# Performance work log

Measured on AMD Instinct MI355X. Metric: run time of the kernel, lower is better.

## Reference

```python
import jax, jax.numpy as jnp
import numpy as np

B, H, W = 4, 512, 512
NOI = 4
LMBDA = 1.0
RHO = 1.0
ALPHA = 1.8
MU = 1.0
C = RHO / (MU + RHO)

QTAB = np.array([16,11,10,16,24,40,51,61,
                 12,12,14,19,26,58,60,55,
                 14,13,16,24,40,57,69,56,
                 14,17,22,29,51,87,80,62,
                 18,22,37,56,68,109,103,77,
                 24,35,55,64,81,104,113,92,
                 49,64,78,87,103,121,120,101,
                 72,92,95,98,112,100,103,99], dtype=np.float32) / 255.0

def _dct_basis():
    xs = 2.0 * np.arange(8) + 1.0
    us = np.pi * np.arange(8) / 16.0
    a = np.ones(8, np.float64); a[0] = 1.0 / np.sqrt(2.0)
    cos = np.cos(np.outer(xs, us)) * a[None, :]          # [x, u]
    F = 0.25 * np.einsum('xu,yv->xyuv', cos, cos).reshape(8, 8, 64)
    return jnp.asarray(F, jnp.float32)

F_DCT = _dct_basis()                                     # [8,8,64]
Q = jnp.asarray(QTAB).reshape(1, 1, 1, 64)

# tf.image kernels (rows index input channel)
K_RGB2YUV = jnp.array([[0.299, -0.14714119, 0.61497538],
                       [0.587, -0.28886916, -0.51496512],
                       [0.114,  0.43601035, -0.10001026]], jnp.float32)
K_YUV2RGB = jnp.array([[1.0, 1.0, 1.0],
                       [0.0, -0.394642334, 2.03206185],
                       [1.13988303, -0.58062185, 0.0]], jnp.float32)

def _dct_blocks(x):
    # x: [B,h*8,w*8] single channel -> [B,h,w,64]; equals stride-8 conv with DCT filters
    b, hh, ww = x.shape
    blk = x.reshape(b, hh // 8, 8, ww // 8, 8)
    return jnp.einsum('bhiwj,ijk->bhwk', blk, F_DCT)

def _idct_blocks(c):
    # c: [B,h,w,64] -> [B,h*8,w*8]; equals depth_to_space + IDCT conv + depth_to_space
    b, hh, ww, _ = c.shape
    img = jnp.einsum('bhwk,ijk->bhiwj', c, F_DCT)
    return img.reshape(b, hh * 8, ww * 8)

def _W(rgb):
    # RGB2JPEG_Coef: rgb -> (y_coefs, u_coefs, v_coefs)
    yuv = rgb @ K_RGB2YUV
    y = yuv[..., 0] - 0.5
    u, v = yuv[..., 1], yuv[..., 2]
    def ds(t):  # 2x2 average pool
        b, hh, ww = t.shape
        return t.reshape(b, hh // 2, 2, ww // 2, 2).mean(axis=(2, 4))
    return (_dct_blocks(y), _dct_blocks(ds(u)), _dct_blocks(ds(v)))

def _Wt(coefs):
    # JPEG_Coef2RGB: (y_c, u_c, v_c) -> rgb
    yc, uc, vc = coefs
    y = jnp.clip(_idct_blocks(yc) + 0.5, 0.0, 1.0)
    def up(t):
        return jnp.repeat(jnp.repeat(t, 2, axis=1), 2, axis=2)
    u = jnp.clip(up(_idct_blocks(uc)), -0.5, 0.5)
    v = jnp.clip(up(_idct_blocks(vc)), -0.5, 0.5)
    yuv = jnp.stack([y, u, v], axis=-1)
    return jnp.clip(yuv @ K_YUV2RGB, 0.0, 1.0)

def _quant_adjust(Wx, r):
    # QuantizationAdjustment: piecewise-best of 3 candidates, elementwise
    y = Wx + C * r
    ry = Q * jnp.round(y / Q)
    sgn_r = jnp.sign(r)
    hqm = Q / 2 - 1.0 / 510.0
    hqp = Q / 2 + 1.0 / 510.0
    def err(d):
        return (MU / 2) * jnp.square(C * r + d) + \
               (RHO / 2) * jnp.square(-MU / (MU + RHO) + Q * jnp.round((y + d) / Q) - y)
    c1 = -sgn_r * jnp.minimum(C * jnp.abs(r), jnp.abs(ry - y - sgn_r * Q * hqm))
    c2 = ry - hqp * Q * jnp.sign(y - ry - C * r) - y
    c3 = -sgn_r * jnp.minimum(C * jnp.abs(r), jnp.abs(ry - y - sgn_r * Q * (1.0 + hqm)))
    best = jnp.where(err(c2) < err(c1), c2, c1)
    return jnp.where(err(c3) < err(best), c3, best)

def _forward(img):
    hh, ww = img.shape[1], img.shape[2]
    # XUpdate: FFT-domain proxy solve with filters [0,1] (vertical / horizontal)
    k1 = jnp.zeros((hh, ww), jnp.float32).at[1, 0].set(1.0)
    k2 = jnp.zeros((hh, ww), jnp.float32).at[0, 1].set(1.0)
    F1 = jnp.fft.rfft2(k1)
    F2 = jnp.fft.rfft2(k2)
    A = 1.0 + LMBDA * (jnp.abs(F1) ** 2 + jnp.abs(F2) ** 2)  # [H, W//2+1]
    def xup(t):
        Tf = jnp.fft.rfft2(t, axes=(1, 2))
        return jnp.fft.irfft2(Tf / A[None, :, :, None], s=(hh, ww), axes=(1, 2))

    Ws = _W(img)
    negC = tuple(Q * jnp.round(w / Q) for w in Ws)
    y = img
    By = negC
    u = tuple(jnp.zeros_like(w) for w in Ws)

    for _ in range(NOI):
        x = xup(y)
        AxplusC = tuple((1.0 - ALPHA) * By[c] - (2.0 - ALPHA) * negC[c] for c in range(3))
        Wx = _W(x)
        r = tuple(-AxplusC[c] - Wx[c] - u[c] for c in range(3))
        Wdz = tuple(_quant_adjust(Wx[c], r[c]) for c in range(3))
        y = x + C * _Wt(r) + _Wt(Wdz)
        By = tuple(Q * jnp.round((Wx[c] + C * r[c] + Wdz[c]) / Q) for c in range(3))
        u = tuple(u[c] + AxplusC[c] + By[c] for c in range(3))

    return xup(y)

def setup_inputs() -> dict:
    key = jax.random.key(0)
    s = jax.random.uniform(key, (B, H, W, 3), dtype=jnp.float32)
    return {"s": s}

def reference(s) -> jnp.ndarray:
    return _forward(s)
```

## Files before the change

kernel.cpp:

```cpp
#include <hip/hip_runtime.h>
#include <math.h>

#define H1 0.49039264020161522f
#define H2 0.46193976625564338f
#define H3 0.41573480615127262f
#define H4 0.35355339059327376f
#define H5 0.27778511650980111f
#define H6 0.19134171618254489f
#define H7 0.09754516100806413f

__device__ __constant__ float cBB[64] = {
  H4,  H1,  H2,  H3,  H4,  H5,  H6,  H7,
  H4,  H3,  H6, -H7, -H4, -H1, -H2, -H5,
  H4,  H5, -H6, -H1, -H4,  H7,  H2,  H3,
  H4,  H7, -H2, -H5,  H4,  H3, -H6, -H1,
  H4, -H7, -H2,  H5,  H4, -H3, -H6,  H1,
  H4, -H5, -H6,  H1, -H4, -H7,  H2, -H3,
  H4, -H3,  H6,  H7, -H4,  H1, -H2,  H5,
  H4, -H1,  H2, -H3,  H4, -H5,  H6, -H7,
};

__device__ __constant__ float cQ[64] = {
  16.f/255.f, 11.f/255.f, 10.f/255.f, 16.f/255.f, 24.f/255.f, 40.f/255.f, 51.f/255.f, 61.f/255.f,
  12.f/255.f, 12.f/255.f, 14.f/255.f, 19.f/255.f, 26.f/255.f, 58.f/255.f, 60.f/255.f, 55.f/255.f,
  14.f/255.f, 13.f/255.f, 16.f/255.f, 24.f/255.f, 40.f/255.f, 57.f/255.f, 69.f/255.f, 56.f/255.f,
  14.f/255.f, 17.f/255.f, 22.f/255.f, 29.f/255.f, 51.f/255.f, 87.f/255.f, 80.f/255.f, 62.f/255.f,
  18.f/255.f, 22.f/255.f, 37.f/255.f, 56.f/255.f, 68.f/255.f, 109.f/255.f, 103.f/255.f, 77.f/255.f,
  24.f/255.f, 35.f/255.f, 55.f/255.f, 64.f/255.f, 81.f/255.f, 104.f/255.f, 113.f/255.f, 92.f/255.f,
  49.f/255.f, 64.f/255.f, 78.f/255.f, 87.f/255.f, 103.f/255.f, 121.f/255.f, 120.f/255.f, 101.f/255.f,
  72.f/255.f, 92.f/255.f, 95.f/255.f, 98.f/255.f, 112.f/255.f, 100.f/255.f, 103.f/255.f, 99.f/255.f,
};

__device__ __forceinline__ float clampf(float x, float lo, float hi) {
    return fminf(fmaxf(x, lo), hi);
}
__device__ __forceinline__ float sgnf(float x) {
    return (x > 0.f) ? 1.f : ((x < 0.f) ? -1.f : 0.f);
}
__device__ __forceinline__ void wave_fence() {
    asm volatile("" ::: "memory");
    __builtin_amdgcn_wave_barrier();
}

__global__ __launch_bounds__(128, 4)
void smooth_jpeg_kernel(const float* __restrict__ s, float* __restrict__ out)
{
    const int t  = threadIdx.x;
    const int l  = t & 63;
    const int w  = t >> 6;
    const int li = l >> 3, lj = l & 7;

    const int tile = blockIdx.x;
    const int bb = tile >> 10;
    const int ti = tile & 1023;
    const int ty = (ti >> 5) * 16;
    const int tx = (ti & 31) * 16;

    __shared__ __align__(16) float BBr[64];
    __shared__ __align__(16) float BBt[64];
    __shared__ __align__(16) float lya[2][128];
    __shared__ __align__(16) float lyb[2][128];
    __shared__ __align__(16) float cuv[2][2][64];
    __shared__ __align__(16) float cst[2][128];
    __shared__ __align__(16) float cb[256];

    if (t < 64) { BBr[t] = cBB[t]; BBt[t] = cBB[(t & 7)*8 + (t >> 3)]; }

    const int gy = ty + w*8 + li;
    int pixo[2];
    float yrv[2], ygv[2], ybv[2];
    #pragma unroll
    for (int k = 0; k < 2; ++k) {
        pixo[k] = ((bb*512 + gy)*512 + (tx + k*8 + lj))*3;
        yrv[k] = s[pixo[k]+0];
        ygv[k] = s[pixo[k]+1];
        ybv[k] = s[pixo[k]+2];
    }

    const float q     = cQ[l];
    const float hqm   = 0.5f*q - (1.0f/510.0f);
    const float qhqm1 = q * hqm;
    const float qhqm3 = q * (1.0f + hqm);
    const float qhqp  = (0.5f*q + (1.0f/510.0f)) * q;

    const bool pooler = ((l & 9) == 0);

    auto load8 = [](const float* p, float* d) {
        float4 a = *reinterpret_cast<const float4*>(p);
        float4 c = *reinterpret_cast<const float4*>(p + 4);
        d[0]=a.x; d[1]=a.y; d[2]=a.z; d[3]=a.w;
        d[4]=c.x; d[5]=c.y; d[6]=c.z; d[7]=c.w;
    };

    auto phaseA = [&](const float* pr, const float* pg, const float* pb,
                      float* pY, int par) {
        #pragma unroll
        for (int k = 0; k < 2; ++k) {
            float yv = 0.299f*pr[k] + 0.587f*pg[k] + 0.114f*pb[k] - 0.5f;
            float uu = -0.14714119f*pr[k] - 0.28886916f*pg[k] + 0.43601035f*pb[k];
            float vv =  0.61497538f*pr[k] - 0.51496512f*pg[k] - 0.10001026f*pb[k];
            pY[k] = yv;
            float ub = __shfl_xor(uu,1), uc = __shfl_xor(uu,8), ud = __shfl_xor(uu,9);
            float vb = __shfl_xor(vv,1), vc = __shfl_xor(vv,8), vd = __shfl_xor(vv,9);
            if (pooler) {
                int ci = (w*4 + (li>>1))*8 + k*4 + (lj>>1);
                cuv[par][0][ci] = 0.25f * (((uu + ub) + uc) + ud);
                cuv[par][1][ci] = 0.25f * (((vv + vb) + vc) + vd);
            }
        }
    };

    auto fwdAll = [&](const float* pY, float* wy, float& wc, int par) {
        #pragma unroll
        for (int k = 0; k < 2; ++k) lya[w][k*64 + l] = pY[k];
        wave_fence();
        float bt[8]; load8(&BBt[lj*8], bt);
        float rs[2], rsc;
        #pragma unroll
        for (int k = 0; k < 2; ++k) {
            float c8[8]; load8(&lya[w][k*64 + li*8], c8);
            float a = 0.f;
            #pragma unroll
            for (int j = 0; j < 8; ++j) a = fmaf(c8[j], bt[j], a);
            rs[k] = a;
        }
        {
            float c8[8]; load8(&cuv[par][w][li*8], c8);
            float a = 0.f;
            #pragma unroll
            for (int j = 0; j < 8; ++j) a = fmaf(c8[j], bt[j], a);
            rsc = a;
        }
        wave_fence();
        #pragma unroll
        for (int k = 0; k < 2; ++k) lyb[w][k*64 + lj*8 + li] = rs[k];
        cst[w][lj*8 + li] = rsc;
        wave_fence();
        float bu[8]; load8(&BBt[li*8], bu);
        #pragma unroll
        for (int k = 0; k < 2; ++k) {
            float c8[8]; load8(&lyb[w][k*64 + lj*8], c8);
            float a = 0.f;
            #pragma unroll
            for (int i = 0; i < 8; ++i) a = fmaf(c8[i], bu[i], a);
            wy[k] = a;
        }
        {
            float c8[8]; load8(&cst[w][lj*8], c8);
            float a = 0.f;
            #pragma unroll
            for (int i = 0; i < 8; ++i) a = fmaf(c8[i], bu[i], a);
            wc = a;
        }
    };

    auto quant = [&](float wx, float neg, float& byS, float& uuS,
                     float& r_out, float& wz_out) {
        float axc = -0.8f*byS - 0.2f*neg;
        float r   = -axc - wx - uuS;
        float yq  = wx + 0.5f*r;
        float r0  = rintf(yq / q);
        float ry  = q * r0;
        float sgn = sgnf(r);
        float aa  = 0.5f*fabsf(r);
        float b1  = fabsf(ry - yq - sgn*qhqm1);
        float b3  = fabsf(ry - yq - sgn*qhqm3);
        float c1  = -sgn * fminf(aa, b1);
        float c3  = -sgn * fminf(aa, b3);
        float sarg = yq - ry - 0.5f*r;
        float sg2  = sgnf(sarg);
        float c2   = ry - qhqp*sg2 - yq;
        float rint1 = rintf((yq + c1) / q);
        float rint3 = rintf((yq + c3) / q);
        float rint2 = r0;
        float a1 = 0.5f*r + c1;
        float a2 = 0.5f*r + c2;
        float a3 = 0.5f*r + c3;
        float e1 = (-0.5f + q*rint1) - yq;
        float e2 = (-0.5f + q*rint2) - yq;
        float e3 = (-0.5f + q*rint3) - yq;
        float err1 = 0.5f*a1*a1 + 0.5f*e1*e1;
        float err2 = 0.5f*a2*a2 + 0.5f*e2*e2;
        float err3 = 0.5f*a3*a3 + 0.5f*e3*e3;
        bool p2 = err2 < err1;
        float best = p2 ? c2 : c1;
        float ebst = p2 ? err2 : err1;
        float rbst = p2 ? rint2 : rint1;
        bool p3 = err3 < ebst;
        float wdz  = p3 ? c3 : best;
        float rwin = p3 ? rint3 : rbst;
        r_out  = r;
        wz_out = wdz;
        byS = q * rwin;
        uuS = (uuS + axc) + byS;
    };

    auto invAll = [&](const float* rY, const float* wzY, float rC, float wzC,
                      float* accR, float* accW) {
        #pragma unroll
        for (int k = 0; k < 2; ++k) { lya[w][k*64 + l] = rY[k]; lyb[w][k*64 + l] = wzY[k]; }
        cst[w][l]      = rC;
        cst[w][64 + l] = wzC;
        wave_fence();
        float bj[8]; load8(&BBr[lj*8], bj);
        float rr[2], rw[2], rcr, rcw;
        #pragma unroll
        for (int k = 0; k < 2; ++k) {
            float c8[8];
            load8(&lya[w][k*64 + li*8], c8);
            float a = 0.f;
            #pragma unroll
            for (int v = 0; v < 8; ++v) a = fmaf(c8[v], bj[v], a);
            rr[k] = a;
            load8(&lyb[w][k*64 + li*8], c8);
            a = 0.f;
            #pragma unroll
            for (int v = 0; v < 8; ++v) a = fmaf(c8[v], bj[v], a);
            rw[k] = a;
        }
        {
            float c8[8];
            load8(&cst[w][li*8], c8);
            float a = 0.f;
            #pragma unroll
            for (int v = 0; v < 8; ++v) a = fmaf(c8[v], bj[v], a);
            rcr = a;
            load8(&cst[w][64 + li*8], c8);
            a = 0.f;
            #pragma unroll
            for (int v = 0; v < 8; ++v) a = fmaf(c8[v], bj[v], a);
            rcw = a;
        }
        wave_fence();
        #pragma unroll
        for (int k = 0; k < 2; ++k) {
            lya[w][k*64 + lj*8 + li] = rr[k];
            lyb[w][k*64 + lj*8 + li] = rw[k];
        }
        cst[w][lj*8 + li]      = rcr;
        cst[w][64 + lj*8 + li] = rcw;
        wave_fence();
        float bi[8]; load8(&BBr[li*8], bi);
        #pragma unroll
        for (int k = 0; k < 2; ++k) {
            float c8[8];
            load8(&lya[w][k*64 + lj*8], c8);
            float a = 0.f;
            #pragma unroll
            for (int u = 0; u < 8; ++u) a = fmaf(c8[u], bi[u], a);
            accR[k] = a;
            load8(&lyb[w][k*64 + lj*8], c8);
            a = 0.f;
            #pragma unroll
            for (int u = 0; u < 8; ++u) a = fmaf(c8[u], bi[u], a);
            accW[k] = a;
        }
        float pcr, pcw;
        {
            float c8[8];
            load8(&cst[w][lj*8], c8);
            float a = 0.f;
            #pragma unroll
            for (int u = 0; u < 8; ++u) a = fmaf(c8[u], bi[u], a);
            pcr = a;
            load8(&cst[w][64 + lj*8], c8);
            a = 0.f;
            #pragma unroll
            for (int u = 0; u < 8; ++u) a = fmaf(c8[u], bi[u], a);
            pcw = a;
        }
        cb[w*64 + l]       = pcr;
        cb[128 + w*64 + l] = pcw;
    };

    float negY[2], byY[2], uY[2];
    float negC, byC, uC;
    {
        float pY[2], wy[2], wc;
        phaseA(yrv, ygv, ybv, pY, 0);
        __syncthreads();
        fwdAll(pY, wy, wc, 0);
        #pragma unroll
        for (int k = 0; k < 2; ++k) {
            negY[k] = q * rintf(wy[k] / q); byY[k] = negY[k]; uY[k] = 0.f;
        }
        negC = q * rintf(wc / q); byC = negC; uC = 0.f;
    }

    #pragma unroll 1
    for (int it = 0; it < 4; ++it) {
        const int par = (it + 1) & 1;
        float xr[2], xg[2], xb[2], pY[2];
        #pragma unroll
        for (int k = 0; k < 2; ++k) {
            xr[k] = yrv[k] * (1.0f/3.0f);
            xg[k] = ygv[k] * (1.0f/3.0f);
            xb[k] = ybv[k] * (1.0f/3.0f);
        }
        phaseA(xr, xg, xb, pY, par);
        __syncthreads();

        float wy[2], wc;
        fwdAll(pY, wy, wc, par);

        float rY[2], wzY[2], rC, wzC;
        #pragma unroll
        for (int k = 0; k < 2; ++k) quant(wy[k], negY[k], byY[k], uY[k], rY[k], wzY[k]);
        quant(wc, negC, byC, uC, rC, wzC);

        float accR[2], accW[2];
        invAll(rY, wzY, rC, wzC, accR, accW);
        __syncthreads();

        #pragma unroll
        for (int k = 0; k < 2; ++k) {
            int kuv = (w*4 + (li>>1))*8 + k*4 + (lj>>1);
            float uR = clampf(cb[kuv],        -0.5f, 0.5f);
            float vR = clampf(cb[64 + kuv],   -0.5f, 0.5f);
            float uW = clampf(cb[128 + kuv],  -0.5f, 0.5f);
            float vW = clampf(cb[192 + kuv],  -0.5f, 0.5f);
            float yR = clampf(accR[k] + 0.5f, 0.f, 1.f);
            float yW = clampf(accW[k] + 0.5f, 0.f, 1.f);
            float rR = clampf(yR + 1.13988303f*vR, 0.f, 1.f);
            float gR = clampf(yR - 0.394642334f*uR - 0.58062185f*vR, 0.f, 1.f);
            float bR = clampf(yR + 2.03206185f*uR, 0.f, 1.f);
            float rW = clampf(yW + 1.13988303f*vW, 0.f, 1.f);
            float gW = clampf(yW - 0.394642334f*uW - 0.58062185f*vW, 0.f, 1.f);
            float bW = clampf(yW + 2.03206185f*uW, 0.f, 1.f);
            yrv[k] = xr[k] + 0.5f*rR + rW;
            ygv[k] = xg[k] + 0.5f*gR + gW;
            ybv[k] = xb[k] + 0.5f*bR + bW;
        }
    }

    #pragma unroll
    for (int k = 0; k < 2; ++k) {
        out[pixo[k]+0] = yrv[k] * (1.0f/3.0f);
        out[pixo[k]+1] = ygv[k] * (1.0f/3.0f);
        out[pixo[k]+2] = ybv[k] * (1.0f/3.0f);
    }
}

extern "C" void kernel_launch(void* const* d_in, const int* in_sizes, int n_in,
                              void* d_out, int out_size, void* d_ws, size_t ws_size,
                              hipStream_t stream) {
    const float* s = (const float*)d_in[0];
    float* out = (float*)d_out;
    smooth_jpeg_kernel<<<dim3(4096), dim3(128), 0, stream>>>(s, out);
}
```

Before: 39.57 us.

## Interleave r/wdz IDCT data in LDS, hoist DCT bases to registers, use DPP

Stores the residual and dead-zone coefficient planes interleaved as float2 in LDS, so the inverse DCT passes read both with one set of vector loads and one transpose step. The four 8-entry DCT basis rows are loaded into registers once instead of being reloaded from LDS in every transform call. The cross-lane shuffles used for 2x2 chroma pooling are replaced with DPP row operations. This cuts LDS traffic and instruction count, at the cost of 32 extra live registers that may pressure occupancy under launch_bounds(128,4).

```diff
diff --git a/kernel.cpp b/kernel.cpp
--- a/kernel.cpp
+++ b/kernel.cpp
@@ -41,6 +41,12 @@
     asm volatile("" ::: "memory");
     __builtin_amdgcn_wave_barrier();
 }
+template<int CTRL>
+__device__ __forceinline__ float dppf(float x) {
+    int v = __builtin_amdgcn_update_dpp(__float_as_int(x), __float_as_int(x),
+                                        CTRL, 0xF, 0xF, false);
+    return __int_as_float(v);
+}
 
 __global__ __launch_bounds__(128, 4)
 void smooth_jpeg_kernel(const float* __restrict__ s, float* __restrict__ out)
@@ -58,10 +64,11 @@
 
     __shared__ __align__(16) float BBr[64];
     __shared__ __align__(16) float BBt[64];
-    __shared__ __align__(16) float lya[2][128];
-    __shared__ __align__(16) float lyb[2][128];
+    __shared__ __align__(16) float s1buf[2][256];
+    __shared__ __align__(16) float s2buf[2][256];
     __shared__ __align__(16) float cuv[2][2][64];
-    __shared__ __align__(16) float cst[2][128];
+    __shared__ __align__(16) float cs1[2][128];
+    __shared__ __align__(16) float cs2[2][128];
     __shared__ __align__(16) float cb[256];
 
     if (t < 64) { BBr[t] = cBB[t]; BBt[t] = cBB[(t & 7)*8 + (t >> 3)]; }
@@ -91,6 +98,16 @@
         d[0]=a.x; d[1]=a.y; d[2]=a.z; d[3]=a.w;
         d[4]=c.x; d[5]=c.y; d[6]=c.z; d[7]=c.w;
     };
+    auto load8x2 = [](const float2* p, float2* d) {
+        float4 a = *reinterpret_cast<const float4*>(p);
+        float4 b = *reinterpret_cast<const float4*>(p + 2);
+        float4 c = *reinterpret_cast<const float4*>(p + 4);
+        float4 e = *reinterpret_cast<const float4*>(p + 6);
+        d[0]=make_float2(a.x,a.y); d[1]=make_float2(a.z,a.w);
+        d[2]=make_float2(b.x,b.y); d[3]=make_float2(b.z,b.w);
+        d[4]=make_float2(c.x,c.y); d[5]=make_float2(c.z,c.w);
+        d[6]=make_float2(e.x,e.y); d[7]=make_float2(e.z,e.w);
+    };
 
     auto phaseA = [&](const float* pr, const float* pg, const float* pb,
                       float* pY, int par) {
@@ -100,8 +117,12 @@
             float uu = -0.14714119f*pr[k] - 0.28886916f*pg[k] + 0.43601035f*pb[k];
             float vv =  0.61497538f*pr[k] - 0.51496512f*pg[k] - 0.10001026f*pb[k];
             pY[k] = yv;
-            float ub = __shfl_xor(uu,1), uc = __shfl_xor(uu,8), ud = __shfl_xor(uu,9);
-            float vb = __shfl_xor(vv,1), vc = __shfl_xor(vv,8), vd = __shfl_xor(vv,9);
+            float ub = dppf<0xB1>(uu);
+            float uc = dppf<0x128>(uu);
+            float ud = dppf<0xB1>(uc);
+            float vb = dppf<0xB1>(vv);
+            float vc = dppf<0x128>(vv);
+            float vd = dppf<0xB1>(vc);
             if (pooler) {
                 int ci = (w*4 + (li>>1))*8 + k*4 + (lj>>1);
                 cuv[par][0][ci] = 0.25f * (((uu + ub) + uc) + ud);
@@ -110,46 +131,46 @@
         }
     };
 
+    float btR[8], buR[8], bjR[8], biR[8];
+
     auto fwdAll = [&](const float* pY, float* wy, float& wc, int par) {
         #pragma unroll
-        for (int k = 0; k < 2; ++k) lya[w][k*64 + l] = pY[k];
-        wave_fence();
-        float bt[8]; load8(&BBt[lj*8], bt);
+        for (int k = 0; k < 2; ++k) s1buf[w][k*64 + l] = pY[k];
+        wave_fence();
         float rs[2], rsc;
         #pragma unroll
         for (int k = 0; k < 2; ++k) {
-            float c8[8]; load8(&lya[w][k*64 + li*8], c8);
+            float c8[8]; load8(&s1buf[w][k*64 + li*8], c8);
             float a = 0.f;
             #pragma unroll
-            for (int j = 0; j < 8; ++j) a = fmaf(c8[j], bt[j], a);
+            for (int j = 0; j < 8; ++j) a = fmaf(c8[j], btR[j], a);
             rs[k] = a;
         }
         {
             float c8[8]; load8(&cuv[par][w][li*8], c8);
             float a = 0.f;
             #pragma unroll
-            for (int j = 0; j < 8; ++j) a = fmaf(c8[j], bt[j], a);
+            for (int j = 0; j < 8; ++j) a = fmaf(c8[j], btR[j], a);
             rsc = a;
         }
         wave_fence();
         #pragma unroll
-        for (int k = 0; k < 2; ++k) lyb[w][k*64 + lj*8 + li] = rs[k];
-        cst[w][lj*8 + li] = rsc;
-        wave_fence();
-        float bu[8]; load8(&BBt[li*8], bu);
-        #pragma unroll
-        for (int k = 0; k < 2; ++k) {
-            float c8[8]; load8(&lyb[w][k*64 + lj*8], c8);
+        for (int k = 0; k < 2; ++k) s2buf[w][k*64 + lj*8 + li] = rs[k];
+        cs1[w][lj*8 + li] = rsc;
+        wave_fence();
+        #pragma unroll
+        for (int k = 0; k < 2; ++k) {
+            float c8[8]; load8(&s2buf[w][k*64 + lj*8], c8);
             float a = 0.f;
             #pragma unroll
-            for (int i = 0; i < 8; ++i) a = fmaf(c8[i], bu[i], a);
+            for (int i = 0; i < 8; ++i) a = fmaf(c8[i], buR[i], a);
             wy[k] = a;
         }
         {
-            float c8[8]; load8(&cst[w][lj*8], c8);
+            float c8[8]; load8(&cs1[w][lj*8], c8);
             float a = 0.f;
             #pragma unroll
-            for (int i = 0; i < 8; ++i) a = fmaf(c8[i], bu[i], a);
+            for (int i = 0; i < 8; ++i) a = fmaf(c8[i], buR[i], a);
             wc = a;
         }
     };
@@ -197,80 +218,64 @@
 
     auto invAll = [&](const float* rY, const float* wzY, float rC, float wzC,
                       float* accR, float* accW) {
-        #pragma unroll
-        for (int k = 0; k < 2; ++k) { lya[w][k*64 + l] = rY[k]; lyb[w][k*64 + l] = wzY[k]; }
-        cst[w][l]      = rC;
-        cst[w][64 + l] = wzC;
-        wave_fence();
-        float bj[8]; load8(&BBr[lj*8], bj);
-        float rr[2], rw[2], rcr, rcw;
-        #pragma unroll
-        for (int k = 0; k < 2; ++k) {
-            float c8[8];
-            load8(&lya[w][k*64 + li*8], c8);
-            float a = 0.f;
-            #pragma unroll
-            for (int v = 0; v < 8; ++v) a = fmaf(c8[v], bj[v], a);
-            rr[k] = a;
-            load8(&lyb[w][k*64 + li*8], c8);
-            a = 0.f;
-            #pragma unroll
-            for (int v = 0; v < 8; ++v) a = fmaf(c8[v], bj[v], a);
-            rw[k] = a;
+        float2* p1 = reinterpret_cast<float2*>(s1buf[w]);
+        float2* c1 = reinterpret_cast<float2*>(cs1[w]);
+        #pragma unroll
+        for (int k = 0; k < 2; ++k) p1[k*64 + l] = make_float2(rY[k], wzY[k]);
+        c1[l] = make_float2(rC, wzC);
+        wave_fence();
+        float2 rr[2], rcc;
+        #pragma unroll
+        for (int k = 0; k < 2; ++k) {
+            float2 c8[8]; load8x2(&p1[k*64 + li*8], c8);
+            float ar = 0.f, aw = 0.f;
+            #pragma unroll
+            for (int v = 0; v < 8; ++v) {
+                ar = fmaf(c8[v].x, bjR[v], ar);
+                aw = fmaf(c8[v].y, bjR[v], aw);
+            }
+            rr[k] = make_float2(ar, aw);
         }
         {
-            float c8[8];
-            load8(&cst[w][li*8], c8);
-            float a = 0.f;
-            #pragma unroll
-            for (int v = 0; v < 8; ++v) a = fmaf(c8[v], bj[v], a);
-            rcr = a;
-            load8(&cst[w][64 + li*8], c8);
-            a = 0.f;
-            #pragma unroll
-            for (int v = 0; v < 8; ++v) a = fmaf(c8[v], bj[v], a);
-            rcw = a;
-        }
-        wave_fence();
-        #pragma unroll
-        for (int k = 0; k < 2; ++k) {
-            lya[w][k*64 + lj*8 + li] = rr[k];
-            lyb[w][k*64 + lj*8 + li] = rw[k];
-        }
-        cst[w][lj*8 + li]      = rcr;
-        cst[w][64 + lj*8 + li] = rcw;
-        wave_fence();
-        float bi[8]; load8(&BBr[li*8], bi);
-        #pragma unroll
-        for (int k = 0; k < 2; ++k) {
-            float c8[8];
-            load8(&lya[w][k*64 + lj*8], c8);
-            float a = 0.f;
-            #pragma unroll
-            for (int u = 0; u < 8; ++u) a = fmaf(c8[u], bi[u], a);
-            accR[k] = a;
-            load8(&lyb[w][k*64 + lj*8], c8);
-            a = 0.f;
-            #pragma unroll
-            for (int u = 0; u < 8; ++u) a = fmaf(c8[u], bi[u], a);
-            accW[k] = a;
-        }
-        float pcr, pcw;
+            float2 c8[8]; load8x2(&c1[li*8], c8);
+            float ar = 0.f, aw = 0.f;
+            #pragma unroll
+            for (int v = 0; v < 8; ++v) {
+                ar = fmaf(c8[v].x, bjR[v], ar);
+                aw = fmaf(c8[v].y, bjR[v], aw);
+            }
+            rcc = make_float2(ar, aw);
+        }
+        wave_fence();
+        float2* p2  = reinterpret_cast<float2*>(s2buf[w]);
+        float2* c2p = reinterpret_cast<float2*>(cs2[w]);
+        #pragma unroll
+        for (int k = 0; k < 2; ++k) p2[k*64 + lj*8 + li] = rr[k];
+        c2p[lj*8 + li] = rcc;
+        wave_fence();
+        #pragma unroll
+        for (int k = 0; k < 2; ++k) {
+            float2 c8[8]; load8x2(&p2[k*64 + lj*8], c8);
+            float ar = 0.f, aw = 0.f;
+            #pragma unroll
+            for (int u = 0; u < 8; ++u) {
+                ar = fmaf(c8[u].x, biR[u], ar);
+                aw = fmaf(c8[u].y, biR[u], aw);
+            }
+            accR[k] = ar;
+            accW[k] = aw;
+        }
         {
-            float c8[8];
-            load8(&cst[w][lj*8], c8);
-            float a = 0.f;
-            #pragma unroll
-            for (int u = 0; u < 8; ++u) a = fmaf(c8[u], bi[u], a);
-            pcr = a;
-            load8(&cst[w][64 + lj*8], c8);
-            a = 0.f;
-            #pragma unroll
-            for (int u = 0; u < 8; ++u) a = fmaf(c8[u], bi[u], a);
-            pcw = a;
-        }
-        cb[w*64 + l]       = pcr;
-        cb[128 + w*64 + l] = pcw;
+            float2 c8[8]; load8x2(&c2p[lj*8], c8);
+            float ar = 0.f, aw = 0.f;
+            #pragma unroll
+            for (int u = 0; u < 8; ++u) {
+                ar = fmaf(c8[u].x, biR[u], ar);
+                aw = fmaf(c8[u].y, biR[u], aw);
+            }
+            cb[w*64 + l]       = ar;
+            cb[128 + w*64 + l] = aw;
+        }
     };
 
     float negY[2], byY[2], uY[2];
@@ -279,6 +284,10 @@
         float pY[2], wy[2], wc;
         phaseA(yrv, ygv, ybv, pY, 0);
         __syncthreads();
+        load8(&BBt[lj*8], btR);
+        load8(&BBt[li*8], buR);
+        load8(&BBr[lj*8], bjR);
+        load8(&BBr[li*8], biR);
         fwdAll(pY, wy, wc, 0);
         #pragma unroll
         for (int k = 0; k < 2; ++k) {
```

After: 41.05 us. 3.7% more time.
